# Kernel tuning notes

Hardware: AMD Instinct MI355X
Metric: run time of the kernel (lower is better)

The kernel has to match this reference:

```python
import jax, jax.numpy as jnp
import numpy as np

# ---- config mirroring DetectionPostProcessV1 init + quant params ----
B, H, W, A, C = 8, 128, 128, 8, 8      # batch, feature HxW, anchors/cell, num_classes
STRIDE = 8
IMG_W, IMG_H = 1024, 1024               # image_size
INPUT_SHIFT = 4                          # kInputShift -> in_scale = 1/16
EXP_SHIFT = 4                            # from _gen_exp_table with in_scale 1/16
BOX_THR_INT = 9                          # ceil(0.55 * 2**INPUT_SHIFT)
NMS_THR = 128.0 / 256.0                  # ceil(0.5 * 2**kNmsThresholdShift) / 2**8
NMS_MARGIN = 0.0                         # nms_margin (quantized: ceil(0*16)/16)
PRE_K, POST_K = 1024, 300                # pre-NMS candidates, post_nms_top_k
CLASS_OFFSETS = jnp.zeros((C,), jnp.int32)
CLASS_SEP = 4096.0                       # coordinate offset for class-aware NMS


def setup_inputs() -> dict:
    key = jax.random.key(0)
    k1, _ = jax.random.split(key)
    # int8 repr of quantized head outputs (stored as int32 for jax indexing)
    data = jax.random.randint(k1, (B, A * (4 + C), H, W), -128, 128, dtype=jnp.int32)
    # grid anchors: 8 sizes per cell, stride-8 feature map
    sizes = np.array([16, 24, 32, 48, 64, 96, 128, 192], np.float32)
    ys = (np.arange(H, dtype=np.float32) + 0.5) * STRIDE
    xs = (np.arange(W, dtype=np.float32) + 0.5) * STRIDE
    cy, cx = np.meshgrid(ys, xs, indexing="ij")
    cx, cy = cx[..., None], cy[..., None]              # [H,W,1]
    w = np.broadcast_to(sizes, (H, W, A))
    h = np.broadcast_to(sizes, (H, W, A))
    anchors = np.stack([cx - w / 2, cy - h / 2, cx + w / 2, cy + h / 2], -1)
    anchors = jnp.asarray(anchors.reshape(-1, 4).astype(np.float32))  # [N,4] matches [H,W,A] flatten order
    # integer exp table, exactly as _gen_exp_table
    in_scale = 1.0 / (1 << INPUT_SHIFT)
    idx = np.arange(-128, 128, dtype=np.float32) * in_scale
    ev = np.exp(idx)
    exp_table = jnp.asarray(np.round(ev * (1 << EXP_SHIFT)).astype(np.int32))
    return {"data": data, "anchors": anchors, "exp_table": exp_table}


def _post_process(data, anchors, exp_table):
    N = H * W * A
    # [B, A*(4+C), H, W] -> [B, N, 4+C]
    x = data.reshape(B, A, 4 + C, H, W).transpose(0, 3, 4, 1, 2).reshape(B, N, 4 + C)
    box_d = x[..., :4]
    scores_i = x[..., 4:] + CLASS_OFFSETS                      # int scores with class offsets
    # decode: dx,dy via fixed-point shift; dw,dh via int exp table lookup
    dxy = box_d[..., :2].astype(jnp.float32) / (1 << INPUT_SHIFT)
    expv = exp_table[box_d[..., 2:4] + 128].astype(jnp.float32) / (1 << EXP_SHIFT)
    ctr = (anchors[:, :2] + anchors[:, 2:]) * 0.5              # [N,2]
    wh = anchors[:, 2:] - anchors[:, :2]
    pc = ctr + dxy * wh                                        # [B,N,2]
    pwh = wh * expv
    boxes = jnp.concatenate([pc - pwh * 0.5, pc + pwh * 0.5], -1)
    boxes = jnp.clip(boxes, 0.0, jnp.array([IMG_W, IMG_H, IMG_W, IMG_H], jnp.float32))
    # score filter
    best = scores_i.max(-1)
    label = scores_i.argmax(-1).astype(jnp.int32)
    valid = best >= BOX_THR_INT
    score = best.astype(jnp.float32) / (1 << INPUT_SHIFT)
    sc_masked = jnp.where(valid, score, -1e9)
    topv, topi = jax.lax.top_k(sc_masked, PRE_K)               # [B,PRE_K]
    bk = jnp.take_along_axis(boxes, topi[..., None], 1)        # [B,PRE_K,4]
    lk = jnp.take_along_axis(label, topi, 1)
    vk = topv > -1e8
    # class-aware NMS via coordinate offset trick
    ob = bk + lk[..., None].astype(jnp.float32) * CLASS_SEP
    area = (ob[..., 2] - ob[..., 0]) * (ob[..., 3] - ob[..., 1])
    lt = jnp.maximum(ob[:, :, None, :2], ob[:, None, :, :2])
    rb = jnp.minimum(ob[:, :, None, 2:], ob[:, None, :, 2:])
    whi = jnp.clip(rb - lt, 0.0)
    inter = whi[..., 0] * whi[..., 1]
    iou = inter / (area[:, :, None] + area[:, None, :] - inter + 1e-9)  # [B,PRE_K,PRE_K]
    idxr = jnp.arange(PRE_K)

    def body(i, sup):
        alive_i = ~jnp.take(sup, i, axis=1)                    # [B]
        iou_i = jnp.take(iou, i, axis=1)                       # [B,PRE_K]
        s_i = jnp.take(topv, i, axis=1)[:, None]
        cond = (alive_i[:, None] & (iou_i > NMS_THR)
                & (topv <= s_i - NMS_MARGIN) & (idxr > i)[None, :])
        return sup | cond

    sup = jax.lax.fori_loop(0, PRE_K, body, ~vk)
    keep = vk & ~sup
    fs = jnp.where(keep, topv, -1e9)
    outv, outi = jax.lax.top_k(fs, POST_K)
    boxes_out = jnp.take_along_axis(bk, outi[..., None], 1)
    labels = jnp.take_along_axis(lk, outi, 1)
    ok = outv > -1e8
    boxes_out = jnp.where(ok[..., None], boxes_out, 0.0)       # [B,POST_K,4]
    scores_out = jnp.where(ok, outv, 0.0)                      # [B,POST_K]
    labels_out = jnp.where(ok, labels, -1)                     # [B,POST_K]
    return boxes_out, scores_out, labels_out


def reference(data, anchors, exp_table):
    return _post_process(data, anchors, exp_table)
```

## Files before the change

kernel.cpp:

```cpp
#include <hip/hip_runtime.h>
#include <stdint.h>

#define Bb 8
#define PREK 1024
#define POSTK 300
#define NBIN 120
#define NCHUNK 512

__device__ __forceinline__ float clampb(float v){ return fminf(fmaxf(v, 0.0f), 1024.0f); }

__global__ void __launch_bounds__(256) k1_scores(const int* __restrict__ data,
                                                 unsigned short* __restrict__ sc16,
                                                 int* __restrict__ chist){
    int blk = blockIdx.x;
    int b = blk >> 7, h = blk & 127;
    int tid = threadIdx.x;
    int a = tid >> 5, wg = tid & 31;
    int w = wg << 2;
    const int* p = data + (((size_t)(b*96 + a*12 + 4)) << 14) + (h << 7) + w;
    int4 m = *(const int4*)p;
    int4 lb = make_int4(0,0,0,0);
#pragma unroll
    for (int c = 1; c < 8; ++c){
        int4 v = *(const int4*)(p + ((size_t)c << 14));
        if (v.x > m.x){ m.x = v.x; lb.x = c; }
        if (v.y > m.y){ m.y = v.y; lb.y = c; }
        if (v.z > m.z){ m.z = v.z; lb.z = c; }
        if (v.w > m.w){ m.w = v.w; lb.w = c; }
    }
    ushort4 st;
    st.x = (unsigned short)(((m.x + 128) << 8) | lb.x);
    st.y = (unsigned short)(((m.y + 128) << 8) | lb.y);
    st.z = (unsigned short)(((m.z + 128) << 8) | lb.z);
    st.w = (unsigned short)(((m.w + 128) << 8) | lb.w);
    *(ushort4*)(sc16 + (((size_t)(b*8 + a)) << 14) + (h << 7) + w) = st;

    __shared__ int hist[4][NBIN];
    for (int i = tid; i < 4*NBIN; i += 256) ((int*)hist)[i] = 0;
    __syncthreads();
    int q = wg >> 3;
    if (m.x >= 9) atomicAdd(&hist[q][m.x-9], 1);
    if (m.y >= 9) atomicAdd(&hist[q][m.y-9], 1);
    if (m.z >= 9) atomicAdd(&hist[q][m.z-9], 1);
    if (m.w >= 9) atomicAdd(&hist[q][m.w-9], 1);
    __syncthreads();
    int* cb = chist + ((size_t)(b*NCHUNK + h*4)) * NBIN;
    for (int i = tid; i < 4*NBIN; i += 256) cb[i] = ((int*)hist)[i];
}

__global__ void __launch_bounds__(1024) k2_select(int* __restrict__ chist, int* __restrict__ gt,
                                                  int* __restrict__ Tb_, int* __restrict__ dmeta){
    int b = blockIdx.x, tid = threadIdx.x;
    __shared__ int part[8][NBIN];
    __shared__ int hs[NBIN];
    __shared__ int suf[128];
    __shared__ int Tsh;
    __shared__ int sb[512];
    if (tid == 0) Tsh = -1;
    const int* cb = chist + (size_t)b * NCHUNK * NBIN;
    if (tid < 8*NBIN){
        int g = tid / NBIN, bin = tid - g*NBIN;
        int s = 0;
        const int* p2 = cb + (size_t)g*64*NBIN + bin;
#pragma unroll 8
        for (int ch = 0; ch < 64; ++ch) s += p2[(size_t)ch * NBIN];
        part[g][bin] = s;
    }
    __syncthreads();
    if (tid < NBIN){
        int s = 0;
#pragma unroll
        for (int g = 0; g < 8; ++g) s += part[g][tid];
        hs[tid] = s;
    }
    __syncthreads();
    int hbin = 0;
    if (tid < 128){
        hbin = (tid < NBIN) ? hs[tid] : 0;
        suf[tid] = hbin;
    }
    __syncthreads();
    for (int off = 1; off < 128; off <<= 1){
        int v = 0;
        if (tid < 128 && tid + off < 128) v = suf[tid + off];
        __syncthreads();
        if (tid < 128) suf[tid] += v;
        __syncthreads();
    }
    if (tid < NBIN){
        gt[b*128 + tid] = suf[tid] - hbin;
        if (suf[tid] >= PREK) atomicMax(&Tsh, tid);
    }
    __syncthreads();
    int T = Tsh > 0 ? Tsh : 0;
    if (tid == 0) Tb_[b] = T;
    dmeta[b*PREK + tid] = -1;
    for (int abin = T; abin < NBIN; ++abin){
        int* basep = chist + (size_t)(b*NCHUNK) * NBIN + abin;
        int v = 0;
        if (tid < 512){ v = basep[(size_t)tid * NBIN]; sb[tid] = v; }
        __syncthreads();
        for (int off = 1; off < 512; off <<= 1){
            int a2 = 0;
            if (tid < 512 && tid >= off) a2 = sb[tid - off];
            __syncthreads();
            if (tid < 512) sb[tid] += a2;
            __syncthreads();
        }
        if (tid < 512) basep[(size_t)tid * NBIN] = sb[tid] - v;
        __syncthreads();
    }
}

__global__ void __launch_bounds__(256) k3_rank(const unsigned short* __restrict__ sc16,
                                               const int* __restrict__ chist,
                                               const int* __restrict__ gt, const int* __restrict__ Tb_,
                                               const int* __restrict__ data,
                                               const float* __restrict__ anchors,
                                               const int* __restrict__ etab,
                                               float4* __restrict__ dbox, int* __restrict__ dmeta){
    int blk = blockIdx.x;
    int b = blk >> 9, ci = blk & 511;
    int tid = threadIdx.x;
    int h = ci >> 2, w0 = (ci & 3) << 5;
    __shared__ unsigned short sc[256];
    __shared__ int wcnt[4][NBIN];
    if (tid < 64){
        int a = tid & 7, wq = tid >> 3;
        ushort4 v4 = *(const ushort4*)(sc16 + (((size_t)(b*8 + a)) << 14) + (h << 7) + w0 + (wq << 2));
        sc[(wq*4 + 0)*8 + a] = v4.x;
        sc[(wq*4 + 1)*8 + a] = v4.y;
        sc[(wq*4 + 2)*8 + a] = v4.z;
        sc[(wq*4 + 3)*8 + a] = v4.w;
    }
    for (int i = tid; i < 4*NBIN; i += 256) ((int*)wcnt)[i] = 0;
    int T = Tb_[b];
    __syncthreads();
    unsigned short v = sc[tid];
    int s = (int)(v >> 8) - 128;
    int bin = s - 9;
    bool qual = (bin >= T);
    int wv = tid >> 6, lane = tid & 63;
    if (qual) atomicAdd(&wcnt[wv][bin], 1);
    __syncthreads();
    int myeq = 0;
    {
        unsigned long long low = (1ull << lane) - 1ull;
        for (int vb = T; vb < NBIN; ++vb){
            unsigned long long bal = __ballot(qual && bin == vb);
            if (!bal) continue;
            if (qual && bin == vb) myeq = __popcll(bal & low);
        }
    }
    if (!qual) return;
    int cross = 0;
    for (int w2 = 0; w2 < wv; ++w2) cross += wcnt[w2][bin];
    int rank = gt[b*128 + bin] + chist[((size_t)(b*NCHUNK) + ci)*NBIN + bin] + cross + myeq;
    if (rank < PREK){
        int n = ci*256 + tid;
        int a = n & 7, wc = (n >> 3) & 127;
        const int* p = data + (((size_t)(b*96 + a*12)) << 14) + (h << 7) + wc;
        int d0 = p[0], d1 = p[1 << 14], d2 = p[2 << 14], d3 = p[3 << 14];
        float4 an = ((const float4*)anchors)[n];
        float cx = __fmul_rn(__fadd_rn(an.x, an.z), 0.5f);
        float cy = __fmul_rn(__fadd_rn(an.y, an.w), 0.5f);
        float wx = __fsub_rn(an.z, an.x), wy = __fsub_rn(an.w, an.y);
        float dx = __fmul_rn((float)d0, 0.0625f), dy = __fmul_rn((float)d1, 0.0625f);
        float ex = __fmul_rn((float)etab[d2 + 128], 0.0625f);
        float ey = __fmul_rn((float)etab[d3 + 128], 0.0625f);
        float pcx = __fadd_rn(cx, __fmul_rn(dx, wx));
        float pcy = __fadd_rn(cy, __fmul_rn(dy, wy));
        float hx = __fmul_rn(__fmul_rn(wx, ex), 0.5f);
        float hy = __fmul_rn(__fmul_rn(wy, ey), 0.5f);
        float x1 = clampb(__fsub_rn(pcx, hx)), y1 = clampb(__fsub_rn(pcy, hy));
        float x2 = clampb(__fadd_rn(pcx, hx)), y2 = clampb(__fadd_rn(pcy, hy));
        dbox[b*PREK + rank] = make_float4(x1, y1, x2, y2);
        dmeta[b*PREK + rank] = (int)v;
    }
}

template<int NG>
__device__ __forceinline__ void nms_reg(const float* __restrict__ X1, const float* __restrict__ Y1,
                                        const float* __restrict__ X2, const float* __restrict__ Y2,
                                        const float* __restrict__ AR,
                                        int base, int M, int lane, unsigned char* __restrict__ KEEP){
    float rx1[NG], ry1[NG], rx2[NG], ry2[NG], rar[NG];
#pragma unroll
    for (int g = 0; g < NG; ++g){
        int r = g*64 + lane;
        int ad = base + ((r < M) ? r : 0);
        rx1[g]=X1[ad]; ry1[g]=Y1[ad]; rx2[g]=X2[ad]; ry2[g]=Y2[ad]; rar[g]=AR[ad];
    }
    unsigned long long mk[NG][NG];
#pragma unroll
    for (int g = 0; g < NG; ++g)
#pragma unroll
        for (int c = 0; c < NG; ++c) mk[g][c] = 0ull;

#pragma unroll
    for (int jw = 0; jw < NG; ++jw){
        if (jw*64 < M){
            int limj = M - jw*64; if (limj > 64) limj = 64;
#pragma unroll 4
            for (int jl = 0; jl < 64; ++jl){
                if (jl < limj){
                    float jx1 = __shfl(rx1[jw], jl);
                    float jy1 = __shfl(ry1[jw], jl);
                    float jx2 = __shfl(rx2[jw], jl);
                    float jy2 = __shfl(ry2[jw], jl);
                    float jar = __fmul_rn(__fsub_rn(jx2, jx1), __fsub_rn(jy2, jy1));
#pragma unroll
                    for (int g = 0; g < NG; ++g){
                        if (g > jw) continue;
                        bool jgi = (g < jw) ? true : (lane < jl);
                        float wx = fmaxf(__fsub_rn(fminf(rx2[g], jx2), fmaxf(rx1[g], jx1)), 0.0f);
                        float wy = fmaxf(__fsub_rn(fminf(ry2[g], jy2), fmaxf(ry1[g], jy1)), 0.0f);
                        float inter = __fmul_rn(wx, wy);
                        float den = __fadd_rn(__fsub_rn(__fadd_rn(rar[g], jar), inter), 1e-9f);
                        bool o = (__fdiv_rn(inter, den) > 0.5f) && jgi;
                        mk[g][jw] |= o ? (1ull << jl) : 0ull;
                    }
                }
            }
        }
    }

    unsigned long long rem[NG];
#pragma unroll
    for (int g = 0; g < NG; ++g) rem[g] = 0ull;
#pragma unroll
    for (int iw = 0; iw < NG; ++iw){
        if (iw*64 < M){
            int limi = M - iw*64; if (limi > 64) limi = 64;
#pragma unroll 4
            for (int il = 0; il < 64; ++il){
                if (il < limi){
                    unsigned long long msk = ((rem[iw] >> il) & 1ull) ? 0ull : ~0ull;
#pragma unroll
                    for (int w = iw; w < NG; ++w){
                        unsigned long long rw = __shfl(mk[iw][w], il);
                        rem[w] |= rw & msk;
                    }
                }
            }
        }
    }
#pragma unroll
    for (int g = 0; g < NG; ++g){
        int r = g*64 + lane;
        unsigned long long rg = rem[g];
        if (r < M) KEEP[base + r] = (unsigned char)(((rg >> lane) & 1ull) ^ 1ull);
    }
}

__global__ void __launch_bounds__(512, 1) k45_nms_out(const float4* __restrict__ dbox,
                                                      const int* __restrict__ dmeta,
                                                      float* __restrict__ out){
    int b = blockIdx.x, tid = threadIdx.x, lane = tid & 63, wv = tid >> 6;
    __shared__ float X1[1024], Y1[1024], X2[1024], Y2[1024], AR[1024];
    __shared__ unsigned char KEEP[1024];
    __shared__ int wq[8][8], wq2[8][8];
    __shared__ int cbs[8], ccn[8];
    __shared__ int wcn[8];
    __shared__ int pbase;

    int v0 = dmeta[b*PREK + tid];
    int v1 = dmeta[b*PREK + 512 + tid];
    float4 bb0 = dbox[b*PREK + tid];
    float4 bb1 = dbox[b*PREK + 512 + tid];
    bool valid0 = (v0 >= 0), valid1 = (v1 >= 0);
    int lc0 = valid0 ? (v0 & 255) : -1;
    int lc1 = valid1 ? (v1 & 255) : -1;
    KEEP[tid] = 0; KEEP[tid + 512] = 0;
    if (tid == 0) pbase = 0;
    int win0 = 0, win1 = 0;
#pragma unroll
    for (int c = 0; c < 8; ++c){
        unsigned long long bal0 = __ballot(lc0 == c);
        unsigned long long bal1 = __ballot(lc1 == c);
        if (lane == 0){ wq[wv][c] = __popcll(bal0); wq2[wv][c] = __popcll(bal1); }
        if (lc0 == c) win0 = __popcll(bal0 & ((1ull << lane) - 1ull));
        if (lc1 == c) win1 = __popcll(bal1 & ((1ull << lane) - 1ull));
    }
    __syncthreads();
    if (tid < 8){
        int run = 0;
        for (int w2 = 0; w2 < 8; ++w2){ int t = wq[w2][tid];  wq[w2][tid]  = run; run += t; }
        for (int w2 = 0; w2 < 8; ++w2){ int t = wq2[w2][tid]; wq2[w2][tid] = run; run += t; }
        ccn[tid] = run;
    }
    __syncthreads();
    if (tid == 0){
        int run = 0;
        for (int c = 0; c < 8; ++c){ cbs[c] = run; run += ccn[c]; }
    }
    __syncthreads();
    int p0 = 0, p1 = 0;
    if (valid0){
        p0 = cbs[lc0] + wq[wv][lc0] + win0;
        float off = (float)(lc0 << 12);
        float ox1 = __fadd_rn(bb0.x, off), oy1 = __fadd_rn(bb0.y, off);
        float ox2 = __fadd_rn(bb0.z, off), oy2 = __fadd_rn(bb0.w, off);
        X1[p0] = ox1; Y1[p0] = oy1; X2[p0] = ox2; Y2[p0] = oy2;
        AR[p0] = __fmul_rn(__fsub_rn(ox2, ox1), __fsub_rn(oy2, oy1));
    }
    if (valid1){
        p1 = cbs[lc1] + wq2[wv][lc1] + win1;
        float off = (float)(lc1 << 12);
        float ox1 = __fadd_rn(bb1.x, off), oy1 = __fadd_rn(bb1.y, off);
        float ox2 = __fadd_rn(bb1.z, off), oy2 = __fadd_rn(bb1.w, off);
        X1[p1] = ox1; Y1[p1] = oy1; X2[p1] = ox2; Y2[p1] = oy2;
        AR[p1] = __fmul_rn(__fsub_rn(ox2, ox1), __fsub_rn(oy2, oy1));
    }
    __syncthreads();

    {
        int M = ccn[wv], base = cbs[wv];
        if (M > 0){
            if (M <= 128)      nms_reg<2>(X1, Y1, X2, Y2, AR, base, M, lane, KEEP);
            else if (M <= 192) nms_reg<3>(X1, Y1, X2, Y2, AR, base, M, lane, KEEP);
            else if (M <= 256) nms_reg<4>(X1, Y1, X2, Y2, AR, base, M, lane, KEEP);
            else {
                for (int m = lane; m < M; m += 64) KEEP[base+m] = 0;
                for (int i = 0; i < M; ++i){
                    if (KEEP[base+i]) continue;
                    float xi1 = X1[base+i], yi1 = Y1[base+i];
                    float xi2 = X2[base+i], yi2 = Y2[base+i], ai = AR[base+i];
                    for (int j = i + 1 + lane; j < M; j += 64){
                        if (KEEP[base+j]) continue;
                        float wx = fmaxf(__fsub_rn(fminf(xi2, X2[base+j]), fmaxf(xi1, X1[base+j])), 0.0f);
                        float wy = fmaxf(__fsub_rn(fminf(yi2, Y2[base+j]), fmaxf(yi1, Y1[base+j])), 0.0f);
                        float inter = __fmul_rn(wx, wy);
                        float den = __fadd_rn(__fsub_rn(__fadd_rn(ai, AR[base+j]), inter), 1e-9f);
                        if (__fdiv_rn(inter, den) > 0.5f) KEEP[base+j] = 1;
                    }
                }
                for (int m = lane; m < M; m += 64) KEEP[base+m] ^= 1;
            }
        }
    }
    __syncthreads();

    float* boxes  = out;
    float* scores = out + Bb*POSTK*4;
    float* labs   = out + Bb*POSTK*5;
#pragma unroll
    for (int pass = 0; pass < 2; ++pass){
        bool vld   = pass ? valid1 : valid0;
        int  pp    = pass ? p1 : p0;
        int  lcc   = pass ? lc1 : lc0;
        int  vv    = pass ? v1 : v0;
        float4 bbb = pass ? bb1 : bb0;
        bool kp = vld && (KEEP[pp] != 0);
        unsigned long long bal = __ballot(kp);
        if (lane == 0) wcn[wv] = __popcll(bal);
        __syncthreads();
        if (tid == 0){
            int r = pbase;
            for (int w2 = 0; w2 < 8; ++w2){ int t = wcn[w2]; wcn[w2] = r; r += t; }
            pbase = r;
        }
        __syncthreads();
        int pos = wcn[wv] + __popcll(bal & ((1ull << lane) - 1ull));
        if (kp && pos < POSTK){
            float sval = __fmul_rn((float)((vv >> 8) - 128), 0.0625f);
            int o = (b*POSTK + pos)*4;
            boxes[o+0] = bbb.x; boxes[o+1] = bbb.y; boxes[o+2] = bbb.z; boxes[o+3] = bbb.w;
            scores[b*POSTK + pos] = sval;
            labs[b*POSTK + pos] = (float)lcc;
        }
        __syncthreads();
    }
    int tot = pbase < POSTK ? pbase : POSTK;
    if (tid >= tot && tid < POSTK){
        int o = (b*POSTK + tid)*4;
        boxes[o+0] = 0.f; boxes[o+1] = 0.f; boxes[o+2] = 0.f; boxes[o+3] = 0.f;
        scores[b*POSTK + tid] = 0.f;
        labs[b*POSTK + tid] = -1.0f;
    }
}

extern "C" void kernel_launch(void* const* d_in, const int* in_sizes, int n_in,
                              void* d_out, int out_size, void* d_ws, size_t ws_size,
                              hipStream_t stream) {
    const int*   data    = (const int*)d_in[0];
    const float* anchors = (const float*)d_in[1];
    const int*   etab    = (const int*)d_in[2];
    float* out = (float*)d_out;

    char* ws = (char*)d_ws;
    size_t off = 0;
    auto alloc = [&](size_t bytes)->char*{ char* p = ws + off; off += (bytes + 255) & ~(size_t)255; return p; };
    unsigned short* sc16 = (unsigned short*)alloc((size_t)Bb*8*16384*2);
    int* chist           = (int*)alloc((size_t)Bb*NCHUNK*NBIN*4);
    int* gt              = (int*)alloc((size_t)Bb*128*4);
    int* Tb_             = (int*)alloc((size_t)Bb*4);
    float4* dbox         = (float4*)alloc((size_t)Bb*PREK*16);
    int* dmeta           = (int*)alloc((size_t)Bb*PREK*4);
    (void)ws_size; (void)in_sizes; (void)n_in; (void)out_size;

    k1_scores<<<Bb*128, 256, 0, stream>>>(data, sc16, chist);
    k2_select<<<Bb, 1024, 0, stream>>>(chist, gt, Tb_, dmeta);
    k3_rank<<<Bb*NCHUNK, 256, 0, stream>>>(sc16, chist, gt, Tb_, data, anchors, etab, dbox, dmeta);
    k45_nms_out<<<Bb, 512, 0, stream>>>(dbox, dmeta, out);
}
```

Measured before the change: 143.9 us.

## Fuse selection, ranking, decode and NMS into one per-batch kernel

Replaces the per-chunk histogram, the separate prefix-scan kernel and the rank kernel. A global histogram is now built with atomics, and a single 1024-thread block per batch scans all 131072 scores, ranks and decodes the top candidates, then runs NMS and writes the output. The aim is to cut launch count and the heavy per-chunk scans through global memory. The cost is that each batch's whole selection loop, 128 iterations per group of 4 bins, runs on only 8 blocks, which risks serialisation and low occupancy.

Measured after the change: 232.9 us. 61.8% more time.

```diff
diff --git a/kernel.cpp b/kernel.cpp
--- a/kernel.cpp
+++ b/kernel.cpp
@@ -2,16 +2,16 @@
 #include <stdint.h>
 
 #define Bb 8
+#define NN 131072
 #define PREK 1024
 #define POSTK 300
 #define NBIN 120
-#define NCHUNK 512
 
 __device__ __forceinline__ float clampb(float v){ return fminf(fmaxf(v, 0.0f), 1024.0f); }
 
 __global__ void __launch_bounds__(256) k1_scores(const int* __restrict__ data,
                                                  unsigned short* __restrict__ sc16,
-                                                 int* __restrict__ chist){
+                                                 int* __restrict__ ghist){
     int blk = blockIdx.x;
     int b = blk >> 7, h = blk & 127;
     int tid = threadIdx.x;
@@ -28,57 +28,124 @@
         if (v.z > m.z){ m.z = v.z; lb.z = c; }
         if (v.w > m.w){ m.w = v.w; lb.w = c; }
     }
-    ushort4 st;
-    st.x = (unsigned short)(((m.x + 128) << 8) | lb.x);
-    st.y = (unsigned short)(((m.y + 128) << 8) | lb.y);
-    st.z = (unsigned short)(((m.z + 128) << 8) | lb.z);
-    st.w = (unsigned short)(((m.w + 128) << 8) | lb.w);
-    *(ushort4*)(sc16 + (((size_t)(b*8 + a)) << 14) + (h << 7) + w) = st;
-
-    __shared__ int hist[4][NBIN];
-    for (int i = tid; i < 4*NBIN; i += 256) ((int*)hist)[i] = 0;
-    __syncthreads();
-    int q = wg >> 3;
-    if (m.x >= 9) atomicAdd(&hist[q][m.x-9], 1);
-    if (m.y >= 9) atomicAdd(&hist[q][m.y-9], 1);
-    if (m.z >= 9) atomicAdd(&hist[q][m.z-9], 1);
-    if (m.w >= 9) atomicAdd(&hist[q][m.w-9], 1);
-    __syncthreads();
-    int* cb = chist + ((size_t)(b*NCHUNK + h*4)) * NBIN;
-    for (int i = tid; i < 4*NBIN; i += 256) cb[i] = ((int*)hist)[i];
+    __shared__ unsigned short st[1024];
+    __shared__ int hist[NBIN];
+    for (int i = tid; i < NBIN; i += 256) hist[i] = 0;
+    st[(w+0)*8 + a] = (unsigned short)(((m.x + 128) << 8) | lb.x);
+    st[(w+1)*8 + a] = (unsigned short)(((m.y + 128) << 8) | lb.y);
+    st[(w+2)*8 + a] = (unsigned short)(((m.z + 128) << 8) | lb.z);
+    st[(w+3)*8 + a] = (unsigned short)(((m.w + 128) << 8) | lb.w);
+    __syncthreads();
+    if (m.x >= 9) atomicAdd(&hist[m.x-9], 1);
+    if (m.y >= 9) atomicAdd(&hist[m.y-9], 1);
+    if (m.z >= 9) atomicAdd(&hist[m.z-9], 1);
+    if (m.w >= 9) atomicAdd(&hist[m.w-9], 1);
+    ushort4* dst = (ushort4*)(sc16 + (((size_t)b) << 17) + (h << 10));
+    dst[tid] = ((const ushort4*)st)[tid];
+    __syncthreads();
+    if (tid < NBIN && hist[tid]) atomicAdd(&ghist[(b << 7) + tid], hist[tid]);
 }
 
-__global__ void __launch_bounds__(1024) k2_select(int* __restrict__ chist, int* __restrict__ gt,
-                                                  int* __restrict__ Tb_, int* __restrict__ dmeta){
-    int b = blockIdx.x, tid = threadIdx.x;
-    __shared__ int part[8][NBIN];
-    __shared__ int hs[NBIN];
-    __shared__ int suf[128];
+template<int NG>
+__device__ __forceinline__ void nms_reg(const float* __restrict__ X1, const float* __restrict__ Y1,
+                                        const float* __restrict__ X2, const float* __restrict__ Y2,
+                                        const float* __restrict__ AR,
+                                        int base, int M, int lane, unsigned char* __restrict__ KEEP){
+    float rx1[NG], ry1[NG], rx2[NG], ry2[NG], rar[NG];
+#pragma unroll
+    for (int g = 0; g < NG; ++g){
+        int r = g*64 + lane;
+        int ad = base + ((r < M) ? r : 0);
+        rx1[g]=X1[ad]; ry1[g]=Y1[ad]; rx2[g]=X2[ad]; ry2[g]=Y2[ad]; rar[g]=AR[ad];
+    }
+    unsigned long long mk[NG][NG];
+#pragma unroll
+    for (int g = 0; g < NG; ++g)
+#pragma unroll
+        for (int c = 0; c < NG; ++c) mk[g][c] = 0ull;
+#pragma unroll
+    for (int jw = 0; jw < NG; ++jw){
+        if (jw*64 < M){
+            int limj = M - jw*64; if (limj > 64) limj = 64;
+#pragma unroll 4
+            for (int jl = 0; jl < 64; ++jl){
+                if (jl < limj){
+                    float jx1 = __shfl(rx1[jw], jl);
+                    float jy1 = __shfl(ry1[jw], jl);
+                    float jx2 = __shfl(rx2[jw], jl);
+                    float jy2 = __shfl(ry2[jw], jl);
+                    float jar = __fmul_rn(__fsub_rn(jx2, jx1), __fsub_rn(jy2, jy1));
+#pragma unroll
+                    for (int g = 0; g < NG; ++g){
+                        if (g > jw) continue;
+                        bool jgi = (g < jw) ? true : (lane < jl);
+                        float wx = fmaxf(__fsub_rn(fminf(rx2[g], jx2), fmaxf(rx1[g], jx1)), 0.0f);
+                        float wy = fmaxf(__fsub_rn(fminf(ry2[g], jy2), fmaxf(ry1[g], jy1)), 0.0f);
+                        float inter = __fmul_rn(wx, wy);
+                        float den = __fadd_rn(__fsub_rn(__fadd_rn(rar[g], jar), inter), 1e-9f);
+                        bool o = (__fdiv_rn(inter, den) > 0.5f) && jgi;
+                        mk[g][jw] |= o ? (1ull << jl) : 0ull;
+                    }
+                }
+            }
+        }
+    }
+    unsigned long long rem[NG];
+#pragma unroll
+    for (int g = 0; g < NG; ++g) rem[g] = 0ull;
+#pragma unroll
+    for (int iw = 0; iw < NG; ++iw){
+        if (iw*64 < M){
+            int limi = M - iw*64; if (limi > 64) limi = 64;
+#pragma unroll 4
+            for (int il = 0; il < 64; ++il){
+                if (il < limi){
+                    unsigned long long msk = ((rem[iw] >> il) & 1ull) ? 0ull : ~0ull;
+#pragma unroll
+                    for (int w = iw; w < NG; ++w){
+                        unsigned long long rw = __shfl(mk[iw][w], il);
+                        rem[w] |= rw & msk;
+                    }
+                }
+            }
+        }
+    }
+#pragma unroll
+    for (int g = 0; g < NG; ++g){
+        int r = g*64 + lane;
+        if (r < M) KEEP[base + r] = (unsigned char)(((rem[g] >> lane) & 1ull) ^ 1ull);
+    }
+}
+
+__global__ void __launch_bounds__(1024) kB(const unsigned short* __restrict__ sc16,
+                                           const int* __restrict__ ghist,
+                                           const int* __restrict__ data,
+                                           const float* __restrict__ anchors,
+                                           const int* __restrict__ etab,
+                                           float* __restrict__ out){
+    int b = blockIdx.x, tid = threadIdx.x, lane = tid & 63, wv = tid >> 6;
+    __shared__ int cntX[2048*4];
+    __shared__ int ridx[PREK];
+    __shared__ unsigned short rsc[PREK];
+    __shared__ int hist[128], gt[128], suf[128];
     __shared__ int Tsh;
-    __shared__ int sb[512];
+    __shared__ int wq[16][8];
+    __shared__ int ccn[8], cbs[8];
+    __shared__ int wcn[16];
+    __shared__ int totS;
+
+    float* X1 = (float*)cntX;
+    float* Y1 = X1 + 1024; float* X2 = Y1 + 1024; float* Y2 = X2 + 1024;
+    float* AR = Y2 + 1024;
+    unsigned char* KEEP = (unsigned char*)(AR + 1024);
+
+    const unsigned short* sb = sc16 + (((size_t)b) << 17);
+
     if (tid == 0) Tsh = -1;
-    const int* cb = chist + (size_t)b * NCHUNK * NBIN;
-    if (tid < 8*NBIN){
-        int g = tid / NBIN, bin = tid - g*NBIN;
-        int s = 0;
-        const int* p2 = cb + (size_t)g*64*NBIN + bin;
-#pragma unroll 8
-        for (int ch = 0; ch < 64; ++ch) s += p2[(size_t)ch * NBIN];
-        part[g][bin] = s;
-    }
-    __syncthreads();
-    if (tid < NBIN){
-        int s = 0;
-#pragma unroll
-        for (int g = 0; g < 8; ++g) s += part[g][tid];
-        hs[tid] = s;
-    }
-    __syncthreads();
-    int hbin = 0;
-    if (tid < 128){
-        hbin = (tid < NBIN) ? hs[tid] : 0;
-        suf[tid] = hbin;
-    }
+    if (tid < 128) hist[tid] = (tid < NBIN) ? ghist[(b << 7) + tid] : 0;
+    ridx[tid] = -1;
+    __syncthreads();
+    if (tid < 128) suf[tid] = hist[tid];
     __syncthreads();
     for (int off = 1; off < 128; off <<= 1){
         int v = 0;
@@ -88,78 +155,66 @@
         __syncthreads();
     }
     if (tid < NBIN){
-        gt[b*128 + tid] = suf[tid] - hbin;
+        gt[tid] = suf[tid] - hist[tid];
         if (suf[tid] >= PREK) atomicMax(&Tsh, tid);
     }
     __syncthreads();
     int T = Tsh > 0 ? Tsh : 0;
-    if (tid == 0) Tb_[b] = T;
-    dmeta[b*PREK + tid] = -1;
-    for (int abin = T; abin < NBIN; ++abin){
-        int* basep = chist + (size_t)(b*NCHUNK) * NBIN + abin;
-        int v = 0;
-        if (tid < 512){ v = basep[(size_t)tid * NBIN]; sb[tid] = v; }
-        __syncthreads();
-        for (int off = 1; off < 512; off <<= 1){
-            int a2 = 0;
-            if (tid < 512 && tid >= off) a2 = sb[tid - off];
+
+    for (int g0 = T; g0 < NBIN; g0 += 4){
+        for (int k = 0; k < 128; ++k){
+            int bin = (int)(sb[(k << 10) + tid] >> 8) - 137;
+#pragma unroll
+            for (int s = 0; s < 4; ++s){
+                unsigned long long bal = __ballot(bin == g0 + s);
+                if (lane == 0) cntX[(((k << 4) + wv) << 2) + s] = __popcll(bal);
+            }
+        }
+        __syncthreads();
+        int orig[8];
+#pragma unroll
+        for (int j = 0; j < 8; ++j) orig[j] = cntX[tid*8 + j];
+        for (int off = 1; off < 2048; off <<= 1){
+            int rd[8];
+#pragma unroll
+            for (int j = 0; j < 8; ++j){
+                int e = 2*tid + (j >> 2), s = j & 3;
+                rd[j] = (e >= off) ? cntX[((e - off) << 2) + s] : 0;
+            }
             __syncthreads();
-            if (tid < 512) sb[tid] += a2;
+#pragma unroll
+            for (int j = 0; j < 8; ++j) cntX[tid*8 + j] += rd[j];
             __syncthreads();
         }
-        if (tid < 512) basep[(size_t)tid * NBIN] = sb[tid] - v;
-        __syncthreads();
-    }
-}
-
-__global__ void __launch_bounds__(256) k3_rank(const unsigned short* __restrict__ sc16,
-                                               const int* __restrict__ chist,
-                                               const int* __restrict__ gt, const int* __restrict__ Tb_,
-                                               const int* __restrict__ data,
-                                               const float* __restrict__ anchors,
-                                               const int* __restrict__ etab,
-                                               float4* __restrict__ dbox, int* __restrict__ dmeta){
-    int blk = blockIdx.x;
-    int b = blk >> 9, ci = blk & 511;
-    int tid = threadIdx.x;
-    int h = ci >> 2, w0 = (ci & 3) << 5;
-    __shared__ unsigned short sc[256];
-    __shared__ int wcnt[4][NBIN];
-    if (tid < 64){
-        int a = tid & 7, wq = tid >> 3;
-        ushort4 v4 = *(const ushort4*)(sc16 + (((size_t)(b*8 + a)) << 14) + (h << 7) + w0 + (wq << 2));
-        sc[(wq*4 + 0)*8 + a] = v4.x;
-        sc[(wq*4 + 1)*8 + a] = v4.y;
-        sc[(wq*4 + 2)*8 + a] = v4.z;
-        sc[(wq*4 + 3)*8 + a] = v4.w;
-    }
-    for (int i = tid; i < 4*NBIN; i += 256) ((int*)wcnt)[i] = 0;
-    int T = Tb_[b];
-    __syncthreads();
-    unsigned short v = sc[tid];
-    int s = (int)(v >> 8) - 128;
-    int bin = s - 9;
-    bool qual = (bin >= T);
-    int wv = tid >> 6, lane = tid & 63;
-    if (qual) atomicAdd(&wcnt[wv][bin], 1);
-    __syncthreads();
-    int myeq = 0;
-    {
-        unsigned long long low = (1ull << lane) - 1ull;
-        for (int vb = T; vb < NBIN; ++vb){
-            unsigned long long bal = __ballot(qual && bin == vb);
-            if (!bal) continue;
-            if (qual && bin == vb) myeq = __popcll(bal & low);
-        }
-    }
-    if (!qual) return;
-    int cross = 0;
-    for (int w2 = 0; w2 < wv; ++w2) cross += wcnt[w2][bin];
-    int rank = gt[b*128 + bin] + chist[((size_t)(b*NCHUNK) + ci)*NBIN + bin] + cross + myeq;
-    if (rank < PREK){
-        int n = ci*256 + tid;
-        int a = n & 7, wc = (n >> 3) & 127;
-        const int* p = data + (((size_t)(b*96 + a*12)) << 14) + (h << 7) + wc;
+#pragma unroll
+        for (int j = 0; j < 8; ++j) cntX[tid*8 + j] -= orig[j];
+        __syncthreads();
+        for (int k = 0; k < 128; ++k){
+            int n = (k << 10) + tid;
+            unsigned short v = sb[n];
+            int bin = (int)(v >> 8) - 137;
+#pragma unroll
+            for (int s = 0; s < 4; ++s){
+                unsigned long long bal = __ballot(bin == g0 + s);
+                if (bin == g0 + s){
+                    int myeq = __popcll(bal & ((1ull << lane) - 1ull));
+                    int rank = gt[bin] + cntX[(((k << 4) + wv) << 2) + s] + myeq;
+                    if (rank < PREK){ rsc[rank] = v; ridx[rank] = n; }
+                }
+            }
+        }
+        __syncthreads();
+    }
+
+    int n = ridx[tid];
+    bool valid = (n >= 0);
+    unsigned short v = valid ? rsc[tid] : (unsigned short)0;
+    int lc = valid ? (v & 255) : -1;
+    float sval = valid ? __fmul_rn((float)((int)(v >> 8) - 128), 0.0625f) : 0.0f;
+    float bx1=0.f, by1=0.f, bx2=0.f, by2=0.f;
+    if (valid){
+        int a = n & 7, hh = n >> 10, wc = (n >> 3) & 127;
+        const int* p = data + (((size_t)(b*96 + a*12)) << 14) + (hh << 7) + wc;
         int d0 = p[0], d1 = p[1 << 14], d2 = p[2 << 14], d3 = p[3 << 14];
         float4 an = ((const float4*)anchors)[n];
         float cx = __fmul_rn(__fadd_rn(an.x, an.z), 0.5f);
@@ -172,121 +227,22 @@
         float pcy = __fadd_rn(cy, __fmul_rn(dy, wy));
         float hx = __fmul_rn(__fmul_rn(wx, ex), 0.5f);
         float hy = __fmul_rn(__fmul_rn(wy, ey), 0.5f);
-        float x1 = clampb(__fsub_rn(pcx, hx)), y1 = clampb(__fsub_rn(pcy, hy));
-        float x2 = clampb(__fadd_rn(pcx, hx)), y2 = clampb(__fadd_rn(pcy, hy));
-        dbox[b*PREK + rank] = make_float4(x1, y1, x2, y2);
-        dmeta[b*PREK + rank] = (int)v;
-    }
-}
-
-template<int NG>
-__device__ __forceinline__ void nms_reg(const float* __restrict__ X1, const float* __restrict__ Y1,
-                                        const float* __restrict__ X2, const float* __restrict__ Y2,
-                                        const float* __restrict__ AR,
-                                        int base, int M, int lane, unsigned char* __restrict__ KEEP){
-    float rx1[NG], ry1[NG], rx2[NG], ry2[NG], rar[NG];
-#pragma unroll
-    for (int g = 0; g < NG; ++g){
-        int r = g*64 + lane;
-        int ad = base + ((r < M) ? r : 0);
-        rx1[g]=X1[ad]; ry1[g]=Y1[ad]; rx2[g]=X2[ad]; ry2[g]=Y2[ad]; rar[g]=AR[ad];
-    }
-    unsigned long long mk[NG][NG];
-#pragma unroll
-    for (int g = 0; g < NG; ++g)
-#pragma unroll
-        for (int c = 0; c < NG; ++c) mk[g][c] = 0ull;
-
-#pragma unroll
-    for (int jw = 0; jw < NG; ++jw){
-        if (jw*64 < M){
-            int limj = M - jw*64; if (limj > 64) limj = 64;
-#pragma unroll 4
-            for (int jl = 0; jl < 64; ++jl){
-                if (jl < limj){
-                    float jx1 = __shfl(rx1[jw], jl);
-                    float jy1 = __shfl(ry1[jw], jl);
-                    float jx2 = __shfl(rx2[jw], jl);
-                    float jy2 = __shfl(ry2[jw], jl);
-                    float jar = __fmul_rn(__fsub_rn(jx2, jx1), __fsub_rn(jy2, jy1));
-#pragma unroll
-                    for (int g = 0; g < NG; ++g){
-                        if (g > jw) continue;
-                        bool jgi = (g < jw) ? true : (lane < jl);
-                        float wx = fmaxf(__fsub_rn(fminf(rx2[g], jx2), fmaxf(rx1[g], jx1)), 0.0f);
-                        float wy = fmaxf(__fsub_rn(fminf(ry2[g], jy2), fmaxf(ry1[g], jy1)), 0.0f);
-                        float inter = __fmul_rn(wx, wy);
-                        float den = __fadd_rn(__fsub_rn(__fadd_rn(rar[g], jar), inter), 1e-9f);
-                        bool o = (__fdiv_rn(inter, den) > 0.5f) && jgi;
-                        mk[g][jw] |= o ? (1ull << jl) : 0ull;
-                    }
-                }
-            }
-        }
-    }
-
-    unsigned long long rem[NG];
-#pragma unroll
-    for (int g = 0; g < NG; ++g) rem[g] = 0ull;
-#pragma unroll
-    for (int iw = 0; iw < NG; ++iw){
-        if (iw*64 < M){
-            int limi = M - iw*64; if (limi > 64) limi = 64;
-#pragma unroll 4
-            for (int il = 0; il < 64; ++il){
-                if (il < limi){
-                    unsigned long long msk = ((rem[iw] >> il) & 1ull) ? 0ull : ~0ull;
-#pragma unroll
-                    for (int w = iw; w < NG; ++w){
-                        unsigned long long rw = __shfl(mk[iw][w], il);
-                        rem[w] |= rw & msk;
-                    }
-                }
-            }
-        }
-    }
-#pragma unroll
-    for (int g = 0; g < NG; ++g){
-        int r = g*64 + lane;
-        unsigned long long rg = rem[g];
-        if (r < M) KEEP[base + r] = (unsigned char)(((rg >> lane) & 1ull) ^ 1ull);
-    }
-}
-
-__global__ void __launch_bounds__(512, 1) k45_nms_out(const float4* __restrict__ dbox,
-                                                      const int* __restrict__ dmeta,
-                                                      float* __restrict__ out){
-    int b = blockIdx.x, tid = threadIdx.x, lane = tid & 63, wv = tid >> 6;
-    __shared__ float X1[1024], Y1[1024], X2[1024], Y2[1024], AR[1024];
-    __shared__ unsigned char KEEP[1024];
-    __shared__ int wq[8][8], wq2[8][8];
-    __shared__ int cbs[8], ccn[8];
-    __shared__ int wcn[8];
-    __shared__ int pbase;
-
-    int v0 = dmeta[b*PREK + tid];
-    int v1 = dmeta[b*PREK + 512 + tid];
-    float4 bb0 = dbox[b*PREK + tid];
-    float4 bb1 = dbox[b*PREK + 512 + tid];
-    bool valid0 = (v0 >= 0), valid1 = (v1 >= 0);
-    int lc0 = valid0 ? (v0 & 255) : -1;
-    int lc1 = valid1 ? (v1 & 255) : -1;
-    KEEP[tid] = 0; KEEP[tid + 512] = 0;
-    if (tid == 0) pbase = 0;
-    int win0 = 0, win1 = 0;
+        bx1 = clampb(__fsub_rn(pcx, hx)); by1 = clampb(__fsub_rn(pcy, hy));
+        bx2 = clampb(__fadd_rn(pcx, hx)); by2 = clampb(__fadd_rn(pcy, hy));
+    }
+
+    KEEP[tid] = 0;
+    int win = 0;
 #pragma unroll
     for (int c = 0; c < 8; ++c){
-        unsigned long long bal0 = __ballot(lc0 == c);
-        unsigned long long bal1 = __ballot(lc1 == c);
-        if (lane == 0){ wq[wv][c] = __popcll(bal0); wq2[wv][c] = __popcll(bal1); }
-        if (lc0 == c) win0 = __popcll(bal0 & ((1ull << lane) - 1ull));
-        if (lc1 == c) win1 = __popcll(bal1 & ((1ull << lane) - 1ull));
+        unsigned long long bal = __ballot(lc == c);
+        if (lane == 0) wq[wv][c] = __popcll(bal);
+        if (lc == c) win = __popcll(bal & ((1ull << lane) - 1ull));
     }
     __syncthreads();
     if (tid < 8){
         int run = 0;
-        for (int w2 = 0; w2 < 8; ++w2){ int t = wq[w2][tid];  wq[w2][tid]  = run; run += t; }
-        for (int w2 = 0; w2 < 8; ++w2){ int t = wq2[w2][tid]; wq2[w2][tid] = run; run += t; }
+        for (int w2 = 0; w2 < 16; ++w2){ int t = wq[w2][tid]; wq[w2][tid] = run; run += t; }
         ccn[tid] = run;
     }
     __syncthreads();
@@ -295,26 +251,18 @@
         for (int c = 0; c < 8; ++c){ cbs[c] = run; run += ccn[c]; }
     }
     __syncthreads();
-    int p0 = 0, p1 = 0;
-    if (valid0){
-        p0 = cbs[lc0] + wq[wv][lc0] + win0;
-        float off = (float)(lc0 << 12);
-        float ox1 = __fadd_rn(bb0.x, off), oy1 = __fadd_rn(bb0.y, off);
-        float ox2 = __fadd_rn(bb0.z, off), oy2 = __fadd_rn(bb0.w, off);
-        X1[p0] = ox1; Y1[p0] = oy1; X2[p0] = ox2; Y2[p0] = oy2;
-        AR[p0] = __fmul_rn(__fsub_rn(ox2, ox1), __fsub_rn(oy2, oy1));
-    }
-    if (valid1){
-        p1 = cbs[lc1] + wq2[wv][lc1] + win1;
-        float off = (float)(lc1 << 12);
-        float ox1 = __fadd_rn(bb1.x, off), oy1 = __fadd_rn(bb1.y, off);
-        float ox2 = __fadd_rn(bb1.z, off), oy2 = __fadd_rn(bb1.w, off);
-        X1[p1] = ox1; Y1[p1] = oy1; X2[p1] = ox2; Y2[p1] = oy2;
-        AR[p1] = __fmul_rn(__fsub_rn(ox2, ox1), __fsub_rn(oy2, oy1));
-    }
-    __syncthreads();
-
-    {
+    int pp = 0;
+    if (valid){
+        pp = cbs[lc] + wq[wv][lc] + win;
+        float off = (float)(lc << 12);
+        float ox1 = __fadd_rn(bx1, off), oy1 = __fadd_rn(by1, off);
+        float ox2 = __fadd_rn(bx2, off), oy2 = __fadd_rn(by2, off);
+        X1[pp] = ox1; Y1[pp] = oy1; X2[pp] = ox2; Y2[pp] = oy2;
+        AR[pp] = __fmul_rn(__fsub_rn(ox2, ox1), __fsub_rn(oy2, oy1));
+    }
+    __syncthreads();
+
+    if (wv < 8){
         int M = ccn[wv], base = cbs[wv];
         if (M > 0){
             if (M <= 128)      nms_reg<2>(X1, Y1, X2, Y2, AR, base, M, lane, KEEP);
@@ -341,37 +289,27 @@
     }
     __syncthreads();
 
+    bool kp = valid && (KEEP[pp] != 0);
+    unsigned long long bal = __ballot(kp);
+    if (lane == 0) wcn[wv] = __popcll(bal);
+    __syncthreads();
+    if (tid == 0){
+        int r = 0;
+        for (int w2 = 0; w2 < 16; ++w2){ int t = wcn[w2]; wcn[w2] = r; r += t; }
+        totS = r;
+    }
+    __syncthreads();
+    int pos = wcn[wv] + __popcll(bal & ((1ull << lane) - 1ull));
     float* boxes  = out;
     float* scores = out + Bb*POSTK*4;
     float* labs   = out + Bb*POSTK*5;
-#pragma unroll
-    for (int pass = 0; pass < 2; ++pass){
-        bool vld   = pass ? valid1 : valid0;
-        int  pp    = pass ? p1 : p0;
-        int  lcc   = pass ? lc1 : lc0;
-        int  vv    = pass ? v1 : v0;
-        float4 bbb = pass ? bb1 : bb0;
-        bool kp = vld && (KEEP[pp] != 0);
-        unsigned long long bal = __ballot(kp);
-        if (lane == 0) wcn[wv] = __popcll(bal);
-        __syncthreads();
-        if (tid == 0){
-            int r = pbase;
-            for (int w2 = 0; w2 < 8; ++w2){ int t = wcn[w2]; wcn[w2] = r; r += t; }
-            pbase = r;
-        }
-        __syncthreads();
-        int pos = wcn[wv] + __popcll(bal & ((1ull << lane) - 1ull));
-        if (kp && pos < POSTK){
-            float sval = __fmul_rn((float)((vv >> 8) - 128), 0.0625f);
-            int o = (b*POSTK + pos)*4;
-            boxes[o+0] = bbb.x; boxes[o+1] = bbb.y; boxes[o+2] = bbb.z; boxes[o+3] = bbb.w;
-            scores[b*POSTK + pos] = sval;
-            labs[b*POSTK + pos] = (float)lcc;
-        }
-        __syncthreads();
-    }
-    int tot = pbase < POSTK ? pbase : POSTK;
+    if (kp && pos < POSTK){
+        int o = (b*POSTK + pos)*4;
+        boxes[o+0] = bx1; boxes[o+1] = by1; boxes[o+2] = bx2; boxes[o+3] = by2;
+        scores[b*POSTK + pos] = sval;
+        labs[b*POSTK + pos] = (float)lc;
+    }
+    int tot = totS < POSTK ? totS : POSTK;
     if (tid >= tot && tid < POSTK){
         int o = (b*POSTK + tid)*4;
         boxes[o+0] = 0.f; boxes[o+1] = 0.f; boxes[o+2] = 0.f; boxes[o+3] = 0.f;
@@ -391,16 +329,11 @@
     char* ws = (char*)d_ws;
     size_t off = 0;
     auto alloc = [&](size_t bytes)->char*{ char* p = ws + off; off += (bytes + 255) & ~(size_t)255; return p; };
-    unsigned short* sc16 = (unsigned short*)alloc((size_t)Bb*8*16384*2);
-    int* chist           = (int*)alloc((size_t)Bb*NCHUNK*NBIN*4);
-    int* gt              = (int*)alloc((size_t)Bb*128*4);
-    int* Tb_             = (int*)alloc((size_t)Bb*4);
-    float4* dbox         = (float4*)alloc((size_t)Bb*PREK*16);
-    int* dmeta           = (int*)alloc((size_t)Bb*PREK*4);
+    unsigned short* sc16 = (unsigned short*)alloc((size_t)Bb*NN*2);
+    int* ghist           = (int*)alloc((size_t)Bb*128*4);
     (void)ws_size; (void)in_sizes; (void)n_in; (void)out_size;
 
-    k1_scores<<<Bb*128, 256, 0, stream>>>(data, sc16, chist);
-    k2_select<<<Bb, 1024, 0, stream>>>(chist, gt, Tb_, dmeta);
-    k3_rank<<<Bb*NCHUNK, 256, 0, stream>>>(sc16, chist, gt, Tb_, data, anchors, etab, dbox, dmeta);
-    k45_nms_out<<<Bb, 512, 0, stream>>>(dbox, dmeta, out);
+    hipMemsetAsync(ghist, 0, (size_t)Bb*128*4, stream);
+    k1_scores<<<Bb*128, 256, 0, stream>>>(data, sc16, ghist);
+    kB<<<Bb, 1024, 0, stream>>>(sc16, ghist, data, anchors, etab, out);
 }
```
